# Optimization experiments

Hardware: AMD Instinct MI355X
Metric: run time of the kernel (lower is better)

Reference implementation:

```python
import jax, jax.numpy as jnp
import numpy as np

KERNEL_MUL = 2.0
KERNEL_NUM = 5

def setup_inputs() -> dict:
    key = jax.random.key(0)
    k1, k2 = jax.random.split(key)
    source = jax.random.normal(k1, (4096, 256), dtype=jnp.float32)
    target = jax.random.normal(k2, (4096, 256), dtype=jnp.float32)
    return {"source": source, "target": target}

def reference(source, target):
    B = source.shape[0]
    total = jnp.concatenate([source, target], axis=0)           # [2N, D]
    n = total.shape[0]
    # pairwise squared L2 distances via expansion (same math as
    # ((total0 - total1)**2).sum(2) without the [2N,2N,D] intermediate)
    sq = jnp.sum(total * total, axis=-1)                         # [2N]
    l2 = jnp.maximum(sq[:, None] + sq[None, :] - 2.0 * (total @ total.T), 0.0)  # [2N,2N]
    # bandwidth from data mean of off-diagonal distances (detached in torch via .data)
    bandwidth = jax.lax.stop_gradient(jnp.sum(l2)) / (n * n - n)
    bandwidth = bandwidth / (KERNEL_MUL ** (KERNEL_NUM // 2))
    kernels = jnp.zeros_like(l2)
    for i in range(KERNEL_NUM):
        kernels = kernels + jnp.exp(-l2 / (bandwidth * (KERNEL_MUL ** i)))
    xx = kernels[:B, :B]
    yy = kernels[B:, B:]
    xy = kernels[:B, B:]
    yx = kernels[B:, :B]
    return jnp.mean(xx + yy - xy - yx)
```

## Files before the change

kernel.cpp:

```cpp
#include <hip/hip_runtime.h>


#define NROWS 8192
#define BHALF 4096
#define DDIM  256
#define TILE  128
#define NTILE 64
#define NBLK  2080

typedef __attribute__((ext_vector_type(8))) short bf16x8;
typedef __attribute__((ext_vector_type(4))) float f32x4;
typedef __attribute__((ext_vector_type(2))) float f32x2;
typedef __attribute__((ext_vector_type(4))) unsigned short u16x4;

struct Ws {
  float coef;
  float Spart[256];
  float cpart[256][256];
  float sq[NROWS];
  float part[NBLK];
};

__device__ __forceinline__ unsigned short f2bf(float x) {
  unsigned int u = __builtin_bit_cast(unsigned int, x);
  return (unsigned short)((u + 0x7fffu + ((u >> 16) & 1u)) >> 16);
}

__device__ __forceinline__ const float* row_ptr(const float* src, const float* tgt, int i) {
  return (i < BHALF) ? (src + (size_t)i * DDIM) : (tgt + (size_t)(i - BHALF) * DDIM);
}

__global__ __launch_bounds__(256) void k_prep(const float* __restrict__ src,
                                              const float* __restrict__ tgt,
                                              Ws* __restrict__ ws,
                                              unsigned short* __restrict__ tb,
                                              int conv) {
  __shared__ float cls[4][256];
  __shared__ float sred[4];
  int tid = threadIdx.x, wave = tid >> 6, lane = tid & 63;
  int row0 = blockIdx.x * 32 + wave * 8;
  float c0 = 0.f, c1 = 0.f, c2 = 0.f, c3 = 0.f;
  float s[8];
  #pragma unroll
  for (int r = 0; r < 8; ++r) {
    const float4* rp = (const float4*)row_ptr(src, tgt, row0 + r);
    float4 x = rp[lane];
    if (conv) {
      u16x4 b = { f2bf(x.x), f2bf(x.y), f2bf(x.z), f2bf(x.w) };
      *(u16x4*)&tb[(size_t)(row0 + r) * DDIM + lane * 4] = b;
    }
    c0 += x.x; c1 += x.y; c2 += x.z; c3 += x.w;
    s[r] = x.x * x.x + x.y * x.y + x.z * x.z + x.w * x.w;
  }
  #pragma unroll
  for (int off = 32; off > 0; off >>= 1) {
    #pragma unroll
    for (int r = 0; r < 8; ++r) s[r] += __shfl_xor(s[r], off);
  }
  if (lane == 0) {
    float Sw = 0.f;
    #pragma unroll
    for (int r = 0; r < 8; ++r) { ws->sq[row0 + r] = s[r]; Sw += s[r]; }
    sred[wave] = Sw;
  }
  cls[wave][lane * 4 + 0] = c0;
  cls[wave][lane * 4 + 1] = c1;
  cls[wave][lane * 4 + 2] = c2;
  cls[wave][lane * 4 + 3] = c3;
  __syncthreads();
  ws->cpart[blockIdx.x][tid] = cls[0][tid] + cls[1][tid] + cls[2][tid] + cls[3][tid];
  if (tid == 0) ws->Spart[blockIdx.x] = sred[0] + sred[1] + sred[2] + sred[3];
}

__global__ __launch_bounds__(256) void k_bw(Ws* __restrict__ ws) {
  __shared__ float redm[4], reds[4];
  int tid = threadIdx.x, wave = tid >> 6, lane = tid & 63;
  float mc = 0.f;
  for (int b = 0; b < 256; ++b) mc += ws->cpart[b][tid];
  float p = mc * mc;
  float sp = ws->Spart[tid];
  #pragma unroll
  for (int off = 32; off > 0; off >>= 1) {
    p  += __shfl_xor(p, off);
    sp += __shfl_xor(sp, off);
  }
  if (lane == 0) { redm[wave] = p; reds[wave] = sp; }
  __syncthreads();
  if (tid == 0) {
    float msq = redm[0] + redm[1] + redm[2] + redm[3];
    float S   = reds[0] + reds[1] + reds[2] + reds[3];
    double n = (double)NROWS;
    double sum_l2 = 2.0 * n * (double)S - 2.0 * (double)msq;
    double bw = sum_l2 / (n * n - n) / 4.0;
    ws->coef = (float)(1.4426950408889634 / (16.0 * bw));
  }
}

__device__ __forceinline__ void stage_tiles(const unsigned short* gA,
                                            const unsigned short* gB,
                                            unsigned short* lA, unsigned short* lB,
                                            int kc) {
  #pragma unroll
  for (int t = 0; t < 4; ++t) {
    __builtin_amdgcn_global_load_lds(
        (const __attribute__((address_space(1))) void*)(gA + (size_t)(t * 8) * DDIM + kc * 64),
        (__attribute__((address_space(3))) void*)(lA + (t * 8) * 64), 16, 0, 0);
    __builtin_amdgcn_global_load_lds(
        (const __attribute__((address_space(1))) void*)(gB + (size_t)(t * 8) * DDIM + kc * 64),
        (__attribute__((address_space(3))) void*)(lB + (t * 8) * 64), 16, 0, 0);
  }
}

template <int FAST>
__global__ __launch_bounds__(256, 4) void k_main(const unsigned short* __restrict__ tb,
                                                 const float* __restrict__ src,
                                                 const float* __restrict__ tgt,
                                                 Ws* __restrict__ ws) {
  int idx = blockIdx.x;
  int ti = (int)((129.0 - sqrt(129.0 * 129.0 - 8.0 * (double)idx)) * 0.5);
  while (64 * (ti + 1) - ((ti + 1) * ti) / 2 <= idx) ++ti;
  while (64 * ti - (ti * (ti - 1)) / 2 > idx) --ti;
  int tj = ti + (idx - (64 * ti - (ti * (ti - 1)) / 2));

  __shared__ __align__(16) unsigned short As[TILE * 64];
  __shared__ __align__(16) unsigned short Bs[TILE * 64];
  __shared__ float wsum[4];

  int tid = threadIdx.x;
  int wave = tid >> 6, lane = tid & 63;
  int wm = wave >> 1, wn = wave & 1;
  int lr = lane & 15, q = lane >> 4;
  int Ib = ti * TILE, Jb = tj * TILE;

  float coef = ws->coef;
  float coef2 = 2.f * coef;
  int ibase = Ib + wm * 64;
  int jbase = Jb + wn * 64;
  float nscj[4];
  f32x2 nsci01[4], nsci23[4];
  #pragma unroll
  for (int n = 0; n < 4; ++n) nscj[n] = -ws->sq[jbase + n * 16 + lr] * coef;
  #pragma unroll
  for (int m = 0; m < 4; ++m) {
    nsci01[m] = f32x2{ -ws->sq[ibase + m * 16 + q * 4 + 0] * coef,
                       -ws->sq[ibase + m * 16 + q * 4 + 1] * coef };
    nsci23[m] = f32x2{ -ws->sq[ibase + m * 16 + q * 4 + 2] * coef,
                       -ws->sq[ibase + m * 16 + q * 4 + 3] * coef };
  }

  f32x4 zero = {0.f, 0.f, 0.f, 0.f};
  f32x4 acc[4][4];
  #pragma unroll
  for (int m = 0; m < 4; ++m)
    #pragma unroll
    for (int n = 0; n < 4; ++n) acc[m][n] = zero;

  const unsigned short* gA = nullptr; const unsigned short* gB = nullptr;
  if (FAST) {
    int lrow = lane >> 3;
    int lchk = (lane & 7) ^ lrow;
    gA = tb + (size_t)(Ib + wave * 32 + lrow) * DDIM + lchk * 8;
    gB = tb + (size_t)(Jb + wave * 32 + lrow) * DDIM + lchk * 8;
  }
  int r0 = tid >> 4, c4 = tid & 15;

  #pragma unroll
  for (int kc = 0; kc < 4; ++kc) {
    if (kc) __syncthreads();
    if (FAST) {
      stage_tiles(gA, gB, &As[(wave * 32) * 64], &Bs[(wave * 32) * 64], kc);
    } else {
      #pragma unroll
      for (int rr = 0; rr < 8; ++rr) {
        int row = rr * 16 + r0;
        int sw = ((c4 >> 1) ^ (row & 7)) * 8 + (c4 & 1) * 4;
        float4 va = ((const float4*)row_ptr(src, tgt, Ib + row))[kc * 16 + c4];
        u16x4 ba = { f2bf(va.x), f2bf(va.y), f2bf(va.z), f2bf(va.w) };
        *(u16x4*)&As[row * 64 + sw] = ba;
        float4 vb = ((const float4*)row_ptr(src, tgt, Jb + row))[kc * 16 + c4];
        u16x4 bb = { f2bf(vb.x), f2bf(vb.y), f2bf(vb.z), f2bf(vb.w) };
        *(u16x4*)&Bs[row * 64 + sw] = bb;
      }
    }
    __syncthreads();
    #pragma unroll
    for (int kk = 0; kk < 2; ++kk) {
      int cidx = ((kk * 4 + q) ^ (lr & 7)) << 3;
      bf16x8 af[4], bfr[4];
      #pragma unroll
      for (int m = 0; m < 4; ++m)
        af[m] = *(const bf16x8*)&As[(wm * 64 + m * 16 + lr) * 64 + cidx];
      #pragma unroll
      for (int n = 0; n < 4; ++n)
        bfr[n] = *(const bf16x8*)&Bs[(wn * 64 + n * 16 + lr) * 64 + cidx];
      #pragma unroll
      for (int m = 0; m < 4; ++m)
        #pragma unroll
        for (int n = 0; n < 4; ++n)
          acc[m][n] = __builtin_amdgcn_mfma_f32_16x16x32_bf16(af[m], bfr[n], acc[m][n], 0, 0, 0);
    }
  }

  const f32x2 c2v = { coef2, coef2 };
  f32x2 accA = {0.f, 0.f}, accB = {0.f, 0.f};
  f32x2 accC = {0.f, 0.f}, accD = {0.f, 0.f};
  #pragma unroll
  for (int m = 0; m < 4; ++m) {
    #pragma unroll
    for (int n = 0; n < 4; ++n) {
      f32x4 g = acc[m][n];
      f32x2 bj = { nscj[n], nscj[n] };
      f32x2 b01 = nsci01[m] + bj;
      f32x2 b23 = nsci23[m] + bj;
      f32x2 a01 = f32x2{g[0], g[1]} * c2v + b01;
      f32x2 a23 = f32x2{g[2], g[3]} * c2v + b23;
      f32x2 t0, t1;
      t0.x = __builtin_amdgcn_exp2f(a01.x); t0.y = __builtin_amdgcn_exp2f(a01.y);
      t1.x = __builtin_amdgcn_exp2f(a23.x); t1.y = __builtin_amdgcn_exp2f(a23.y);
      f32x2 p0 = t0 * t0, p1 = t1 * t1;
      f32x2 q0 = p0 * p0, q1 = p1 * p1;
      f32x2 r0v = q0 * q0, r1v = q1 * q1;
      accA += t0 + p0;
      accB += q0 + r0v;
      accA = r0v * r0v + accA;
      accC += t1 + p1;
      accD += q1 + r1v;
      accC = r1v * r1v + accC;
    }
  }
  float lsum = (accA.x + accA.y) + (accB.x + accB.y)
             + (accC.x + accC.y) + (accD.x + accD.y);
  #pragma unroll
  for (int off = 32; off > 0; off >>= 1) lsum += __shfl_xor(lsum, off);
  if (lane == 0) wsum[wave] = lsum;
  __syncthreads();
  if (tid == 0) {
    float tot = wsum[0] + wsum[1] + wsum[2] + wsum[3];
    float sA = (ti < 32) ? 1.f : -1.f;
    float sB = (tj < 32) ? 1.f : -1.f;
    float fac = sA * sB * ((ti == tj) ? 1.f : 2.f);
    ws->part[blockIdx.x] = fac * tot;
  }
}

__global__ __launch_bounds__(256) void k_final(const Ws* __restrict__ ws,
                                               float* __restrict__ out) {
  __shared__ double red[4];
  int tid = threadIdx.x, wave = tid >> 6, lane = tid & 63;
  double s = 0.0;
  for (int i = tid; i < NBLK; i += 256) s += (double)ws->part[i];
  #pragma unroll
  for (int off = 32; off > 0; off >>= 1) s += __shfl_xor(s, off);
  if (lane == 0) red[wave] = s;
  __syncthreads();
  if (tid == 0)
    out[0] = (float)((red[0] + red[1] + red[2] + red[3]) /
                     ((double)BHALF * (double)BHALF));
}

extern "C" void kernel_launch(void* const* d_in, const int* in_sizes, int n_in,
                              void* d_out, int out_size, void* d_ws, size_t ws_size,
                              hipStream_t stream) {
  const float* src = (const float*)d_in[0];
  const float* tgt = (const float*)d_in[1];
  Ws* ws = (Ws*)d_ws;
  float* out = (float*)d_out;

  size_t wsoff = (sizeof(Ws) + 255) & ~(size_t)255;
  size_t need = wsoff + (size_t)NROWS * DDIM * 2;
  bool fast = ws_size >= need;
  unsigned short* tb = fast ? (unsigned short*)((char*)d_ws + wsoff) : nullptr;

  hipLaunchKernelGGL(k_prep, dim3(256), dim3(256), 0, stream, src, tgt, ws, tb,
                     fast ? 1 : 0);
  hipLaunchKernelGGL(k_bw, dim3(1), dim3(256), 0, stream, ws);
  if (fast)
    hipLaunchKernelGGL((k_main<1>), dim3(NBLK), dim3(256), 0, stream, tb, src, tgt, ws);
  else
    hipLaunchKernelGGL((k_main<0>), dim3(NBLK), dim3(256), 0, stream, tb, src, tgt, ws);
  hipLaunchKernelGGL(k_final, dim3(1), dim3(256), 0, stream, ws, out);
}
```

Measured before the change: 107.3 us.

## Fuse prep, bandwidth, Gram tiles and final reduction into one cooperative kernel

Replaces the four-launch sequence (prep, bandwidth, main tile kernel, final reduce) with a single cooperative persistent kernel that uses grid-wide syncs between phases and a grid-stride loop over triangular tiles. Column and squared-norm partial sums are combined with atomics into eight slots that are zeroed by a memset, and diagonal tiles stage only one panel and reuse it for both operands. The intent is to remove launch gaps and the serial single-block bandwidth and final kernels. In exchange it adds two grid barriers and a memset, and the persistent grid may balance tiles less evenly than one block per tile.

```diff
diff --git a/kernel.cpp b/kernel.cpp
--- a/kernel.cpp
+++ b/kernel.cpp
@@ -1,4 +1,7 @@
 #include <hip/hip_runtime.h>
+#include <hip/hip_cooperative_groups.h>
+
+namespace cg = cooperative_groups;
 
 
 #define NROWS 8192
@@ -14,6 +17,8 @@
 typedef __attribute__((ext_vector_type(4))) unsigned short u16x4;
 
 struct Ws {
+  float Ssum8[8];
+  float colsum2[8][256];
   float coef;
   float Spart[256];
   float cpart[256][256];
@@ -28,6 +33,203 @@
 
 __device__ __forceinline__ const float* row_ptr(const float* src, const float* tgt, int i) {
   return (i < BHALF) ? (src + (size_t)i * DDIM) : (tgt + (size_t)(i - BHALF) * DDIM);
+}
+
+__device__ __forceinline__ void stage_panel(const unsigned short* g,
+                                            unsigned short* l, int kc) {
+  #pragma unroll
+  for (int t = 0; t < 4; ++t)
+    __builtin_amdgcn_global_load_lds(
+        (const __attribute__((address_space(1))) void*)(g + (size_t)(t * 8) * DDIM + kc * 64),
+        (__attribute__((address_space(3))) void*)(l + (t * 8) * 64), 16, 0, 0);
+}
+
+__global__ __launch_bounds__(256, 4) void k_all(const float* __restrict__ src,
+                                                const float* __restrict__ tgt,
+                                                Ws* __restrict__ ws,
+                                                unsigned short* __restrict__ tb,
+                                                float* __restrict__ out) {
+  __shared__ __align__(16) unsigned short As[TILE * 64];
+  __shared__ __align__(16) unsigned short Bs[TILE * 64];
+  __shared__ float wsum[4];
+  __shared__ float coefS;
+  __shared__ double dred[4];
+
+  int tid = threadIdx.x, wave = tid >> 6, lane = tid & 63;
+
+  {
+    float (*cls)[256] = (float (*)[256])As;
+    float* sred = (float*)Bs;
+    int W = blockIdx.x * 4 + wave, NW = gridDim.x * 4;
+    float c0 = 0.f, c1 = 0.f, c2 = 0.f, c3 = 0.f, Sw = 0.f;
+    for (int pr = W; pr < NROWS / 2; pr += NW) {
+      #pragma unroll
+      for (int r = 0; r < 2; ++r) {
+        int row = pr * 2 + r;
+        float4 x = ((const float4*)row_ptr(src, tgt, row))[lane];
+        u16x4 b = { f2bf(x.x), f2bf(x.y), f2bf(x.z), f2bf(x.w) };
+        *(u16x4*)&tb[(size_t)row * DDIM + lane * 4] = b;
+        c0 += x.x; c1 += x.y; c2 += x.z; c3 += x.w;
+        float s = x.x * x.x + x.y * x.y + x.z * x.z + x.w * x.w;
+        #pragma unroll
+        for (int off = 32; off > 0; off >>= 1) s += __shfl_xor(s, off);
+        if (lane == 0) { ws->sq[row] = s; Sw += s; }
+      }
+    }
+    cls[wave][lane * 4 + 0] = c0;
+    cls[wave][lane * 4 + 1] = c1;
+    cls[wave][lane * 4 + 2] = c2;
+    cls[wave][lane * 4 + 3] = c3;
+    if (lane == 0) sred[wave] = Sw;
+    __syncthreads();
+    atomicAdd(&ws->colsum2[blockIdx.x & 7][tid],
+              cls[0][tid] + cls[1][tid] + cls[2][tid] + cls[3][tid]);
+    if (tid == 0)
+      atomicAdd(&ws->Ssum8[blockIdx.x & 7], sred[0] + sred[1] + sred[2] + sred[3]);
+    __syncthreads();
+  }
+  cg::this_grid().sync();
+
+  {
+    float mc = 0.f;
+    #pragma unroll
+    for (int k = 0; k < 8; ++k) mc += ws->colsum2[k][tid];
+    float p = mc * mc;
+    #pragma unroll
+    for (int off = 32; off > 0; off >>= 1) p += __shfl_xor(p, off);
+    if (lane == 0) wsum[wave] = p;
+    __syncthreads();
+    if (tid == 0) {
+      float msq = wsum[0] + wsum[1] + wsum[2] + wsum[3];
+      float S = 0.f;
+      #pragma unroll
+      for (int k = 0; k < 8; ++k) S += ws->Ssum8[k];
+      double n = (double)NROWS;
+      double sum_l2 = 2.0 * n * (double)S - 2.0 * (double)msq;
+      double bwv = sum_l2 / (n * n - n) / 4.0;
+      coefS = (float)(1.4426950408889634 / (16.0 * bwv));
+    }
+    __syncthreads();
+  }
+  float coef = coefS;
+  float coef2 = 2.f * coef;
+  int wm = wave >> 1, wn = wave & 1;
+  int lr = lane & 15, q = lane >> 4;
+  int lrow = lane >> 3;
+  int lchk = (lane & 7) ^ lrow;
+  float blocksum = 0.f;
+
+  for (int idx = blockIdx.x; idx < NBLK; idx += gridDim.x) {
+    int ti = (int)((129.0 - sqrt(129.0 * 129.0 - 8.0 * (double)idx)) * 0.5);
+    while (64 * (ti + 1) - ((ti + 1) * ti) / 2 <= idx) ++ti;
+    while (64 * ti - (ti * (ti - 1)) / 2 > idx) --ti;
+    int tj = ti + (idx - (64 * ti - (ti * (ti - 1)) / 2));
+    int Ib = ti * TILE, Jb = tj * TILE;
+    bool diag = (ti == tj);
+
+    int ibase = Ib + wm * 64;
+    int jbase = Jb + wn * 64;
+    float nscj[4];
+    f32x2 nsci01[4], nsci23[4];
+    #pragma unroll
+    for (int n = 0; n < 4; ++n) nscj[n] = -ws->sq[jbase + n * 16 + lr] * coef;
+    #pragma unroll
+    for (int m = 0; m < 4; ++m) {
+      nsci01[m] = f32x2{ -ws->sq[ibase + m * 16 + q * 4 + 0] * coef,
+                         -ws->sq[ibase + m * 16 + q * 4 + 1] * coef };
+      nsci23[m] = f32x2{ -ws->sq[ibase + m * 16 + q * 4 + 2] * coef,
+                         -ws->sq[ibase + m * 16 + q * 4 + 3] * coef };
+    }
+
+    f32x4 zero = {0.f, 0.f, 0.f, 0.f};
+    f32x4 acc[4][4];
+    #pragma unroll
+    for (int m = 0; m < 4; ++m)
+      #pragma unroll
+      for (int n = 0; n < 4; ++n) acc[m][n] = zero;
+
+    const unsigned short* gA = tb + (size_t)(Ib + wave * 32 + lrow) * DDIM + lchk * 8;
+    const unsigned short* gB = tb + (size_t)(Jb + wave * 32 + lrow) * DDIM + lchk * 8;
+    const unsigned short* Bbase = diag ? As : Bs;
+
+    #pragma unroll
+    for (int kc = 0; kc < 4; ++kc) {
+      if (kc) __syncthreads();
+      stage_panel(gA, &As[(wave * 32) * 64], kc);
+      if (!diag) stage_panel(gB, &Bs[(wave * 32) * 64], kc);
+      __syncthreads();
+      #pragma unroll
+      for (int kk = 0; kk < 2; ++kk) {
+        int cidx = ((kk * 4 + q) ^ (lr & 7)) << 3;
+        bf16x8 af[4], bfr[4];
+        #pragma unroll
+        for (int m = 0; m < 4; ++m)
+          af[m] = *(const bf16x8*)&As[(wm * 64 + m * 16 + lr) * 64 + cidx];
+        #pragma unroll
+        for (int n = 0; n < 4; ++n)
+          bfr[n] = *(const bf16x8*)&Bbase[(wn * 64 + n * 16 + lr) * 64 + cidx];
+        #pragma unroll
+        for (int m = 0; m < 4; ++m)
+          #pragma unroll
+          for (int n = 0; n < 4; ++n)
+            acc[m][n] = __builtin_amdgcn_mfma_f32_16x16x32_bf16(af[m], bfr[n], acc[m][n], 0, 0, 0);
+      }
+    }
+
+    const f32x2 c2v = { coef2, coef2 };
+    f32x2 accA = {0.f, 0.f}, accB = {0.f, 0.f};
+    f32x2 accC = {0.f, 0.f}, accD = {0.f, 0.f};
+    #pragma unroll
+    for (int m = 0; m < 4; ++m) {
+      #pragma unroll
+      for (int n = 0; n < 4; ++n) {
+        f32x4 g = acc[m][n];
+        f32x2 bj = { nscj[n], nscj[n] };
+        f32x2 b01 = nsci01[m] + bj;
+        f32x2 b23 = nsci23[m] + bj;
+        f32x2 a01 = f32x2{g[0], g[1]} * c2v + b01;
+        f32x2 a23 = f32x2{g[2], g[3]} * c2v + b23;
+        f32x2 t0, t1;
+        t0.x = __builtin_amdgcn_exp2f(a01.x); t0.y = __builtin_amdgcn_exp2f(a01.y);
+        t1.x = __builtin_amdgcn_exp2f(a23.x); t1.y = __builtin_amdgcn_exp2f(a23.y);
+        f32x2 p0 = t0 * t0, p1 = t1 * t1;
+        f32x2 q0 = p0 * p0, q1 = p1 * p1;
+        f32x2 r0v = q0 * q0, r1v = q1 * q1;
+        accA += t0 + p0;
+        accB += q0 + r0v;
+        accA = r0v * r0v + accA;
+        accC += t1 + p1;
+        accD += q1 + r1v;
+        accC = r1v * r1v + accC;
+      }
+    }
+    float lsum = (accA.x + accA.y) + (accB.x + accB.y)
+               + (accC.x + accC.y) + (accD.x + accD.y);
+    #pragma unroll
+    for (int off = 32; off > 0; off >>= 1) lsum += __shfl_xor(lsum, off);
+    if (lane == 0) wsum[wave] = lsum;
+    __syncthreads();
+    if (tid == 0) {
+      float tot = wsum[0] + wsum[1] + wsum[2] + wsum[3];
+      float sA = (ti < 32) ? 1.f : -1.f;
+      float sB = (tj < 32) ? 1.f : -1.f;
+      blocksum += sA * sB * ((ti == tj) ? 1.f : 2.f) * tot;
+    }
+  }
+  if (tid == 0) ws->part[blockIdx.x] = blocksum;
+  cg::this_grid().sync();
+
+  if (blockIdx.x == 0) {
+    double s = 0.0;
+    for (int i = tid; i < (int)gridDim.x; i += 256) s += (double)ws->part[i];
+    #pragma unroll
+    for (int off = 32; off > 0; off >>= 1) s += __shfl_xor(s, off);
+    if (lane == 0) dred[wave] = s;
+    __syncthreads();
+    if (tid == 0)
+      out[0] = (float)((dred[0] + dred[1] + dred[2] + dred[3]) /
+                       ((double)BHALF * (double)BHALF));
+  }
 }
 
 __global__ __launch_bounds__(256) void k_prep(const float* __restrict__ src,
@@ -91,23 +293,8 @@
     float S   = reds[0] + reds[1] + reds[2] + reds[3];
     double n = (double)NROWS;
     double sum_l2 = 2.0 * n * (double)S - 2.0 * (double)msq;
-    double bw = sum_l2 / (n * n - n) / 4.0;
-    ws->coef = (float)(1.4426950408889634 / (16.0 * bw));
-  }
-}
-
-__device__ __forceinline__ void stage_tiles(const unsigned short* gA,
-                                            const unsigned short* gB,
-                                            unsigned short* lA, unsigned short* lB,
-                                            int kc) {
-  #pragma unroll
-  for (int t = 0; t < 4; ++t) {
-    __builtin_amdgcn_global_load_lds(
-        (const __attribute__((address_space(1))) void*)(gA + (size_t)(t * 8) * DDIM + kc * 64),
-        (__attribute__((address_space(3))) void*)(lA + (t * 8) * 64), 16, 0, 0);
-    __builtin_amdgcn_global_load_lds(
-        (const __attribute__((address_space(1))) void*)(gB + (size_t)(t * 8) * DDIM + kc * 64),
-        (__attribute__((address_space(3))) void*)(lB + (t * 8) * 64), 16, 0, 0);
+    double bwv = sum_l2 / (n * n - n) / 4.0;
+    ws->coef = (float)(1.4426950408889634 / (16.0 * bwv));
   }
 }
 
@@ -168,7 +355,8 @@
   for (int kc = 0; kc < 4; ++kc) {
     if (kc) __syncthreads();
     if (FAST) {
-      stage_tiles(gA, gB, &As[(wave * 32) * 64], &Bs[(wave * 32) * 64], kc);
+      stage_panel(gA, &As[(wave * 32) * 64], kc);
+      stage_panel(gB, &Bs[(wave * 32) * 64], kc);
     } else {
       #pragma unroll
       for (int rr = 0; rr < 8; ++rr) {
@@ -271,12 +459,30 @@
   bool fast = ws_size >= need;
   unsigned short* tb = fast ? (unsigned short*)((char*)d_ws + wsoff) : nullptr;
 
-  hipLaunchKernelGGL(k_prep, dim3(256), dim3(256), 0, stream, src, tgt, ws, tb,
-                     fast ? 1 : 0);
-  hipLaunchKernelGGL(k_bw, dim3(1), dim3(256), 0, stream, ws);
-  if (fast)
-    hipLaunchKernelGGL((k_main<1>), dim3(NBLK), dim3(256), 0, stream, tb, src, tgt, ws);
-  else
-    hipLaunchKernelGGL((k_main<0>), dim3(NBLK), dim3(256), 0, stream, tb, src, tgt, ws);
-  hipLaunchKernelGGL(k_final, dim3(1), dim3(256), 0, stream, ws, out);
-}
+  bool coop_ok = false;
+  if (fast) {
+    int bpc = 0;
+    hipError_t qe = hipOccupancyMaxActiveBlocksPerMultiprocessor(&bpc, k_all, 256, 0);
+    if (qe == hipSuccess && bpc >= 1) {
+      int grid = bpc * 256;
+      if (grid > NBLK) grid = NBLK;
+      hipMemsetAsync(d_ws, 0, 8224, stream);
+      const float* a0 = src; const float* a1 = tgt;
+      Ws* a2 = ws; unsigned short* a3 = tb; float* a4 = out;
+      void* args[] = { &a0, &a1, &a2, &a3, &a4 };
+      hipError_t le = hipLaunchCooperativeKernel((const void*)k_all, dim3(grid),
+                                                 dim3(256), args, 0, stream);
+      coop_ok = (le == hipSuccess);
+    }
+  }
+  if (!coop_ok) {
+    hipLaunchKernelGGL(k_prep, dim3(256), dim3(256), 0, stream, src, tgt, ws, tb,
+                       fast ? 1 : 0);
+    hipLaunchKernelGGL(k_bw, dim3(1), dim3(256), 0, stream, ws);
+    if (fast)
+      hipLaunchKernelGGL((k_main<1>), dim3(NBLK), dim3(256), 0, stream, tb, src, tgt, ws);
+    else
+      hipLaunchKernelGGL((k_main<0>), dim3(NBLK), dim3(256), 0, stream, tb, src, tgt, ws);
+    hipLaunchKernelGGL(k_final, dim3(1), dim3(256), 0, stream, ws, out);
+  }
+}
```

Measured after the change: 239.1 us. +122.8%, slower.

## Split main kernel into producer and consumer waves with double-buffered LDS

Applied to the files above, without the earlier changes.

Doubles the block to 512 threads: four producer waves stage the next K-chunk of the A/B tiles into a second LDS buffer while four consumer waves run MFMAs on the current buffer, then the consumers do the exp epilogue. This is meant to hide global-to-LDS load latency behind matrix math instead of serialising load, sync and compute. In exchange LDS use per block doubles (64 KB), the blocks are larger, and half the waves sit idle during the epilogue, all of which can reduce occupancy.

```diff
diff --git a/kernel.cpp b/kernel.cpp
--- a/kernel.cpp
+++ b/kernel.cpp
@@ -91,28 +91,22 @@
     float S   = reds[0] + reds[1] + reds[2] + reds[3];
     double n = (double)NROWS;
     double sum_l2 = 2.0 * n * (double)S - 2.0 * (double)msq;
-    double bw = sum_l2 / (n * n - n) / 4.0;
-    ws->coef = (float)(1.4426950408889634 / (16.0 * bw));
-  }
-}
-
-__device__ __forceinline__ void stage_tiles(const unsigned short* gA,
-                                            const unsigned short* gB,
-                                            unsigned short* lA, unsigned short* lB,
-                                            int kc) {
-  #pragma unroll
-  for (int t = 0; t < 4; ++t) {
+    double bwv = sum_l2 / (n * n - n) / 4.0;
+    ws->coef = (float)(1.4426950408889634 / (16.0 * bwv));
+  }
+}
+
+__device__ __forceinline__ void stage_panel(const unsigned short* g,
+                                            unsigned short* l, int kc) {
+  #pragma unroll
+  for (int t = 0; t < 4; ++t)
     __builtin_amdgcn_global_load_lds(
-        (const __attribute__((address_space(1))) void*)(gA + (size_t)(t * 8) * DDIM + kc * 64),
-        (__attribute__((address_space(3))) void*)(lA + (t * 8) * 64), 16, 0, 0);
-    __builtin_amdgcn_global_load_lds(
-        (const __attribute__((address_space(1))) void*)(gB + (size_t)(t * 8) * DDIM + kc * 64),
-        (__attribute__((address_space(3))) void*)(lB + (t * 8) * 64), 16, 0, 0);
-  }
+        (const __attribute__((address_space(1))) void*)(g + (size_t)(t * 8) * DDIM + kc * 64),
+        (__attribute__((address_space(3))) void*)(l + (t * 8) * 64), 16, 0, 0);
 }
 
 template <int FAST>
-__global__ __launch_bounds__(256, 4) void k_main(const unsigned short* __restrict__ tb,
+__global__ __launch_bounds__(512, 4) void k_main(const unsigned short* __restrict__ tb,
                                                  const float* __restrict__ src,
                                                  const float* __restrict__ tgt,
                                                  Ws* __restrict__ ws) {
@@ -122,117 +116,151 @@
   while (64 * ti - (ti * (ti - 1)) / 2 > idx) --ti;
   int tj = ti + (idx - (64 * ti - (ti * (ti - 1)) / 2));
 
-  __shared__ __align__(16) unsigned short As[TILE * 64];
-  __shared__ __align__(16) unsigned short Bs[TILE * 64];
-  __shared__ float wsum[4];
+  __shared__ __align__(16) unsigned short As[2][TILE * 64];
+  __shared__ __align__(16) unsigned short Bs[2][TILE * 64];
 
   int tid = threadIdx.x;
   int wave = tid >> 6, lane = tid & 63;
-  int wm = wave >> 1, wn = wave & 1;
+  bool producer = wave >= 4;
+  int Ib = ti * TILE, Jb = tj * TILE;
+
+  int wm = (wave >> 1) & 1, wn = wave & 1;
   int lr = lane & 15, q = lane >> 4;
-  int Ib = ti * TILE, Jb = tj * TILE;
-
-  float coef = ws->coef;
-  float coef2 = 2.f * coef;
-  int ibase = Ib + wm * 64;
-  int jbase = Jb + wn * 64;
+  float coef = 0.f, coef2 = 0.f;
   float nscj[4];
   f32x2 nsci01[4], nsci23[4];
-  #pragma unroll
-  for (int n = 0; n < 4; ++n) nscj[n] = -ws->sq[jbase + n * 16 + lr] * coef;
-  #pragma unroll
-  for (int m = 0; m < 4; ++m) {
-    nsci01[m] = f32x2{ -ws->sq[ibase + m * 16 + q * 4 + 0] * coef,
-                       -ws->sq[ibase + m * 16 + q * 4 + 1] * coef };
-    nsci23[m] = f32x2{ -ws->sq[ibase + m * 16 + q * 4 + 2] * coef,
-                       -ws->sq[ibase + m * 16 + q * 4 + 3] * coef };
-  }
-
-  f32x4 zero = {0.f, 0.f, 0.f, 0.f};
   f32x4 acc[4][4];
-  #pragma unroll
-  for (int m = 0; m < 4; ++m)
-    #pragma unroll
-    for (int n = 0; n < 4; ++n) acc[m][n] = zero;
+  if (!producer) {
+    coef = ws->coef;
+    coef2 = 2.f * coef;
+    int ibase = Ib + wm * 64;
+    int jbase = Jb + wn * 64;
+    #pragma unroll
+    for (int n = 0; n < 4; ++n) nscj[n] = -ws->sq[jbase + n * 16 + lr] * coef;
+    #pragma unroll
+    for (int m = 0; m < 4; ++m) {
+      nsci01[m] = f32x2{ -ws->sq[ibase + m * 16 + q * 4 + 0] * coef,
+                         -ws->sq[ibase + m * 16 + q * 4 + 1] * coef };
+      nsci23[m] = f32x2{ -ws->sq[ibase + m * 16 + q * 4 + 2] * coef,
+                         -ws->sq[ibase + m * 16 + q * 4 + 3] * coef };
+    }
+    f32x4 zero = {0.f, 0.f, 0.f, 0.f};
+    #pragma unroll
+    for (int m = 0; m < 4; ++m)
+      #pragma unroll
+      for (int n = 0; n < 4; ++n) acc[m][n] = zero;
+  }
 
   const unsigned short* gA = nullptr; const unsigned short* gB = nullptr;
-  if (FAST) {
+  int pw = wave - 4;
+  if (FAST && producer) {
     int lrow = lane >> 3;
     int lchk = (lane & 7) ^ lrow;
-    gA = tb + (size_t)(Ib + wave * 32 + lrow) * DDIM + lchk * 8;
-    gB = tb + (size_t)(Jb + wave * 32 + lrow) * DDIM + lchk * 8;
-  }
-  int r0 = tid >> 4, c4 = tid & 15;
-
-  #pragma unroll
-  for (int kc = 0; kc < 4; ++kc) {
-    if (kc) __syncthreads();
+    gA = tb + (size_t)(Ib + pw * 32 + lrow) * DDIM + lchk * 8;
+    gB = tb + (size_t)(Jb + pw * 32 + lrow) * DDIM + lchk * 8;
+  }
+  int ptid = tid - 256;
+  int r0 = ptid >> 4, c4 = ptid & 15;
+
+  if (producer) {
     if (FAST) {
-      stage_tiles(gA, gB, &As[(wave * 32) * 64], &Bs[(wave * 32) * 64], kc);
+      stage_panel(gA, &As[0][(pw * 32) * 64], 0);
+      stage_panel(gB, &Bs[0][(pw * 32) * 64], 0);
     } else {
       #pragma unroll
       for (int rr = 0; rr < 8; ++rr) {
         int row = rr * 16 + r0;
         int sw = ((c4 >> 1) ^ (row & 7)) * 8 + (c4 & 1) * 4;
-        float4 va = ((const float4*)row_ptr(src, tgt, Ib + row))[kc * 16 + c4];
+        float4 va = ((const float4*)row_ptr(src, tgt, Ib + row))[c4];
         u16x4 ba = { f2bf(va.x), f2bf(va.y), f2bf(va.z), f2bf(va.w) };
-        *(u16x4*)&As[row * 64 + sw] = ba;
-        float4 vb = ((const float4*)row_ptr(src, tgt, Jb + row))[kc * 16 + c4];
+        *(u16x4*)&As[0][row * 64 + sw] = ba;
+        float4 vb = ((const float4*)row_ptr(src, tgt, Jb + row))[c4];
         u16x4 bb = { f2bf(vb.x), f2bf(vb.y), f2bf(vb.z), f2bf(vb.w) };
-        *(u16x4*)&Bs[row * 64 + sw] = bb;
+        *(u16x4*)&Bs[0][row * 64 + sw] = bb;
       }
     }
-    __syncthreads();
-    #pragma unroll
-    for (int kk = 0; kk < 2; ++kk) {
-      int cidx = ((kk * 4 + q) ^ (lr & 7)) << 3;
-      bf16x8 af[4], bfr[4];
+  }
+  __syncthreads();
+
+  #pragma unroll
+  for (int kc = 0; kc < 4; ++kc) {
+    int cur = kc & 1;
+    if (producer) {
+      if (kc < 3) {
+        int nxt = cur ^ 1;
+        if (FAST) {
+          stage_panel(gA, &As[nxt][(pw * 32) * 64], kc + 1);
+          stage_panel(gB, &Bs[nxt][(pw * 32) * 64], kc + 1);
+        } else {
+          #pragma unroll
+          for (int rr = 0; rr < 8; ++rr) {
+            int row = rr * 16 + r0;
+            int sw = ((c4 >> 1) ^ (row & 7)) * 8 + (c4 & 1) * 4;
+            float4 va = ((const float4*)row_ptr(src, tgt, Ib + row))[(kc + 1) * 16 + c4];
+            u16x4 ba = { f2bf(va.x), f2bf(va.y), f2bf(va.z), f2bf(va.w) };
+            *(u16x4*)&As[nxt][row * 64 + sw] = ba;
+            float4 vb = ((const float4*)row_ptr(src, tgt, Jb + row))[(kc + 1) * 16 + c4];
+            u16x4 bb = { f2bf(vb.x), f2bf(vb.y), f2bf(vb.z), f2bf(vb.w) };
+            *(u16x4*)&Bs[nxt][row * 64 + sw] = bb;
+          }
+        }
+      }
+    } else {
       #pragma unroll
-      for (int m = 0; m < 4; ++m)
-        af[m] = *(const bf16x8*)&As[(wm * 64 + m * 16 + lr) * 64 + cidx];
-      #pragma unroll
-      for (int n = 0; n < 4; ++n)
-        bfr[n] = *(const bf16x8*)&Bs[(wn * 64 + n * 16 + lr) * 64 + cidx];
-      #pragma unroll
-      for (int m = 0; m < 4; ++m)
+      for (int kk = 0; kk < 2; ++kk) {
+        int cidx = ((kk * 4 + q) ^ (lr & 7)) << 3;
+        bf16x8 af[4], bfr[4];
+        #pragma unroll
+        for (int m = 0; m < 4; ++m)
+          af[m] = *(const bf16x8*)&As[cur][(wm * 64 + m * 16 + lr) * 64 + cidx];
         #pragma unroll
         for (int n = 0; n < 4; ++n)
-          acc[m][n] = __builtin_amdgcn_mfma_f32_16x16x32_bf16(af[m], bfr[n], acc[m][n], 0, 0, 0);
-    }
-  }
-
-  const f32x2 c2v = { coef2, coef2 };
-  f32x2 accA = {0.f, 0.f}, accB = {0.f, 0.f};
-  f32x2 accC = {0.f, 0.f}, accD = {0.f, 0.f};
-  #pragma unroll
-  for (int m = 0; m < 4; ++m) {
-    #pragma unroll
-    for (int n = 0; n < 4; ++n) {
-      f32x4 g = acc[m][n];
-      f32x2 bj = { nscj[n], nscj[n] };
-      f32x2 b01 = nsci01[m] + bj;
-      f32x2 b23 = nsci23[m] + bj;
-      f32x2 a01 = f32x2{g[0], g[1]} * c2v + b01;
-      f32x2 a23 = f32x2{g[2], g[3]} * c2v + b23;
-      f32x2 t0, t1;
-      t0.x = __builtin_amdgcn_exp2f(a01.x); t0.y = __builtin_amdgcn_exp2f(a01.y);
-      t1.x = __builtin_amdgcn_exp2f(a23.x); t1.y = __builtin_amdgcn_exp2f(a23.y);
-      f32x2 p0 = t0 * t0, p1 = t1 * t1;
-      f32x2 q0 = p0 * p0, q1 = p1 * p1;
-      f32x2 r0v = q0 * q0, r1v = q1 * q1;
-      accA += t0 + p0;
-      accB += q0 + r0v;
-      accA = r0v * r0v + accA;
-      accC += t1 + p1;
-      accD += q1 + r1v;
-      accC = r1v * r1v + accC;
-    }
-  }
-  float lsum = (accA.x + accA.y) + (accB.x + accB.y)
-             + (accC.x + accC.y) + (accD.x + accD.y);
-  #pragma unroll
-  for (int off = 32; off > 0; off >>= 1) lsum += __shfl_xor(lsum, off);
-  if (lane == 0) wsum[wave] = lsum;
+          bfr[n] = *(const bf16x8*)&Bs[cur][(wn * 64 + n * 16 + lr) * 64 + cidx];
+        #pragma unroll
+        for (int m = 0; m < 4; ++m)
+          #pragma unroll
+          for (int n = 0; n < 4; ++n)
+            acc[m][n] = __builtin_amdgcn_mfma_f32_16x16x32_bf16(af[m], bfr[n], acc[m][n], 0, 0, 0);
+      }
+    }
+    __syncthreads();
+  }
+
+  float* wsum = (float*)As;
+  if (!producer) {
+    const f32x2 c2v = { coef2, coef2 };
+    f32x2 accA = {0.f, 0.f}, accB = {0.f, 0.f};
+    f32x2 accC = {0.f, 0.f}, accD = {0.f, 0.f};
+    #pragma unroll
+    for (int m = 0; m < 4; ++m) {
+      #pragma unroll
+      for (int n = 0; n < 4; ++n) {
+        f32x4 g = acc[m][n];
+        f32x2 bj = { nscj[n], nscj[n] };
+        f32x2 b01 = nsci01[m] + bj;
+        f32x2 b23 = nsci23[m] + bj;
+        f32x2 a01 = f32x2{g[0], g[1]} * c2v + b01;
+        f32x2 a23 = f32x2{g[2], g[3]} * c2v + b23;
+        f32x2 t0, t1;
+        t0.x = __builtin_amdgcn_exp2f(a01.x); t0.y = __builtin_amdgcn_exp2f(a01.y);
+        t1.x = __builtin_amdgcn_exp2f(a23.x); t1.y = __builtin_amdgcn_exp2f(a23.y);
+        f32x2 p0 = t0 * t0, p1 = t1 * t1;
+        f32x2 q0 = p0 * p0, q1 = p1 * p1;
+        f32x2 r0v = q0 * q0, r1v = q1 * q1;
+        accA += t0 + p0;
+        accB += q0 + r0v;
+        accA = r0v * r0v + accA;
+        accC += t1 + p1;
+        accD += q1 + r1v;
+        accC = r1v * r1v + accC;
+      }
+    }
+    float lsum = (accA.x + accA.y) + (accB.x + accB.y)
+               + (accC.x + accC.y) + (accD.x + accD.y);
+    #pragma unroll
+    for (int off = 32; off > 0; off >>= 1) lsum += __shfl_xor(lsum, off);
+    if (lane == 0) wsum[wave] = lsum;
+  }
   __syncthreads();
   if (tid == 0) {
     float tot = wsum[0] + wsum[1] + wsum[2] + wsum[3];
@@ -275,8 +303,8 @@
                      fast ? 1 : 0);
   hipLaunchKernelGGL(k_bw, dim3(1), dim3(256), 0, stream, ws);
   if (fast)
-    hipLaunchKernelGGL((k_main<1>), dim3(NBLK), dim3(256), 0, stream, tb, src, tgt, ws);
+    hipLaunchKernelGGL((k_main<1>), dim3(NBLK), dim3(512), 0, stream, tb, src, tgt, ws);
   else
-    hipLaunchKernelGGL((k_main<0>), dim3(NBLK), dim3(256), 0, stream, tb, src, tgt, ws);
+    hipLaunchKernelGGL((k_main<0>), dim3(NBLK), dim3(512), 0, stream, tb, src, tgt, ws);
   hipLaunchKernelGGL(k_final, dim3(1), dim3(256), 0, stream, ws, out);
 }
```

Result: slower. 119.8 us (+11.6%).
